# Kernel tuning notes

Measured on AMD Instinct MI355X. Metric: run time of the kernel, lower is better.

## Reference

```python
import jax, jax.numpy as jnp
import numpy as np

B, C, N, M, K = 1, 64, 65536, 65536, 16
H, O = 64, 128  # mlp hidden, out_channels


def setup_inputs() -> dict:
    key = jax.random.key(0)
    ks = jax.random.split(key, 8)
    return {
        "x": jax.random.normal(ks[0], (B, C, N), dtype=jnp.float32),
        "pos": jax.random.normal(ks[1], (B, 3, N), dtype=jnp.float32),
        "support_points": jax.random.normal(ks[2], (B, 3, M), dtype=jnp.float32),
        "W1": jax.random.normal(ks[3], (H, C + 3), dtype=jnp.float32) * 0.05,
        "b1": jax.random.normal(ks[4], (H,), dtype=jnp.float32) * 0.05,
        "W2": jax.random.normal(ks[5], (O, H), dtype=jnp.float32) * 0.05,
        "b2": jax.random.normal(ks[6], (O,), dtype=jnp.float32) * 0.05,
        "indices": jax.random.randint(ks[7], (B, M, K), 0, N, dtype=jnp.int64),
    }


def _gather_points(t, indices):
    # t: [B, C, N], indices: [B, M, K] -> [B, C, M, K]
    b, c, n = t.shape
    m, k = indices.shape[1], indices.shape[2]
    idx = indices.reshape(b, 1, m * k)  # broadcasts over channel dim
    return jnp.take_along_axis(t, idx, axis=2).reshape(b, c, m, k)


def reference(x, pos, support_points, W1, b1, W2, b2, indices):
    # gather neighbor features and positions: [B, C, M, K], [B, 3, M, K]
    feats = _gather_points(x, indices)
    pts = _gather_points(pos, indices) - support_points[:, :, :, None]
    h = jnp.concatenate([feats, pts], axis=1)  # [B, C+3, M, K]
    # shared per-point MLP (1x1 Conv2d == channel contraction)
    h = jnp.einsum("oc,bcmk->bomk", W1, h) + b1[None, :, None, None]
    h = jax.nn.relu(h)
    h = jnp.einsum("oc,bcmk->bomk", W2, h) + b2[None, :, None, None]
    # max-pool over neighborhood K -> [B, O, M]
    return jnp.max(h, axis=3)
```

## Files before the change

### kernel.cpp

```cpp
#include <hip/hip_runtime.h>
#include <hip/hip_bf16.h>

#define NPTS 65536
#define MPTS 65536

typedef __attribute__((ext_vector_type(8))) short bf16x8;
typedef __attribute__((ext_vector_type(4))) float f32x4;

__device__ __forceinline__ float bflo(unsigned int u){ union{unsigned int i; float f;} v; v.i = u<<16; return v.f; }
__device__ __forceinline__ float bfhi(unsigned int u){ union{unsigned int i; float f;} v; v.i = u & 0xffff0000u; return v.f; }
__device__ __forceinline__ unsigned short f2bf(float f){
  union{float f; unsigned int i;} v; v.f=f;
  unsigned int r = v.i + 0x7fffu + ((v.i>>16)&1u);
  return (unsigned short)(r>>16);
}
__device__ __forceinline__ unsigned int pk2f(float a, float b){
  float2 tf; tf.x = a; tf.y = b;
  union { __hip_bfloat162 h; unsigned int u; } c;
  c.h = __float22bfloat162_rn(tf);
  return c.u;
}
__device__ __forceinline__ float swz16(float x){
  return __int_as_float(__builtin_amdgcn_ds_swizzle(__float_as_int(x), 0x401F));
}
__device__ __forceinline__ float red4(f32x4 a){
  return fmaxf(fmaxf(a[0], a[1]), fmaxf(a[2], a[3]));
}

#define MFMA32(a,b,c) __builtin_amdgcn_mfma_f32_16x16x32_bf16((a),(b),(c),0,0,0)

__global__ __launch_bounds__(256) void pack_all(
    const float* __restrict__ x,
    const float* __restrict__ pos,
    const float* __restrict__ sup,
    const float* __restrict__ W1,
    const float* __restrict__ b1,
    const float* __restrict__ W2,
    unsigned short* __restrict__ U,
    unsigned short* __restrict__ W2F,
    float* __restrict__ V) {
  const int t = threadIdx.x;
  if (blockIdx.x >= 1028) {
    const int m = (blockIdx.x - 1028) * 256 + t;
    const float s0 = sup[m], s1 = sup[MPTS + m], s2 = sup[2*MPTS + m];
    #pragma unroll
    for (int cg = 0; cg < 16; ++cg) {
      const float* r0 = W1 + (size_t)(cg*4 + 0)*67 + 64;
      const float* r1 = W1 + (size_t)(cg*4 + 1)*67 + 64;
      const float* r2 = W1 + (size_t)(cg*4 + 2)*67 + 64;
      const float* r3 = W1 + (size_t)(cg*4 + 3)*67 + 64;
      float4 o;
      o.x = r0[0]*s0 + r0[1]*s1 + r0[2]*s2;
      o.y = r1[0]*s0 + r1[1]*s1 + r1[2]*s2;
      o.z = r2[0]*s0 + r2[1]*s1 + r2[2]*s2;
      o.w = r3[0]*s0 + r3[1]*s1 + r3[2]*s2;
      *(float4*)(V + (size_t)m*64 + cg*4) = o;
    }
    return;
  }
  if (blockIdx.x >= 1024) {
    const int gg = (blockIdx.x - 1024) * 256 + t;
    if (gg < 1024) {
      const int g = gg >> 6, lane = gg & 63;
      const int q = lane >> 4, lr = lane & 15;
      const int kt = g >> 3, ot = g & 7;
      #pragma unroll
      for (int j = 0; j < 4; ++j)
        *(unsigned int*)&W2F[gg*8 + 2*j] =
            pk2f(W2[(ot*16 + lr)*64 + kt*32 + q*8 + 2*j],
                 W2[(ot*16 + lr)*64 + kt*32 + q*8 + 2*j + 1]);
    }
    return;
  }
  __shared__ float sx[67][65];
  const int n0 = blockIdx.x * 64;
  #pragma unroll
  for (int i = 0; i < 4; ++i) {
    const int lin = i*256 + t, r = lin >> 4, c4 = (lin & 15) * 4;
    const float4 v = *(const float4*)&x[(size_t)r * NPTS + n0 + c4];
    *(float4*)&sx[r][c4] = v;
  }
  if (t < 48) {
    const int lin = 1024 + t, r = lin >> 4, c4 = (lin & 15) * 4;
    const float4 v = *(const float4*)&pos[(size_t)(r - 64) * NPTS + n0 + c4];
    *(float4*)&sx[r][c4] = v;
  }

  const int lane = t & 63, w = t >> 6, quad = lane >> 4, lr = lane & 15;
  const int col = w * 16 + lr;
  const int n = n0 + col;

  bf16x8 wa[2][4], wt[4];
  #pragma unroll
  for (int kt = 0; kt < 2; ++kt)
    #pragma unroll
    for (int nt = 0; nt < 4; ++nt) {
      const float* r = W1 + (size_t)(nt*16 + lr)*67 + kt*32 + quad*8;
      const float4 a = *(const float4*)r;
      const float4 b = *(const float4*)(r + 4);
      union { unsigned int d[4]; bf16x8 v; } mk;
      mk.d[0] = pk2f(a.x, a.y); mk.d[1] = pk2f(a.z, a.w);
      mk.d[2] = pk2f(b.x, b.y); mk.d[3] = pk2f(b.z, b.w);
      wa[kt][nt] = mk.v;
    }
  #pragma unroll
  for (int nt = 0; nt < 4; ++nt) {
    union { unsigned int d[4]; bf16x8 v; } mk;
    mk.d[0] = 0u; mk.d[1] = 0u; mk.d[2] = 0u; mk.d[3] = 0u;
    if (quad == 0) {
      const float* r = W1 + (size_t)(nt*16 + lr)*67 + 64;
      mk.d[0] = pk2f(r[0], r[1]);
      mk.d[1] = (unsigned int)f2bf(r[2]);
    }
    wt[nt] = mk.v;
  }

  __syncthreads();

  const f32x4 fz = {0.f, 0.f, 0.f, 0.f};
  f32x4 acc[4] = {fz, fz, fz, fz};
  #pragma unroll
  for (int kt = 0; kt < 2; ++kt) {
    const int c0 = kt*32 + quad*8;
    union { unsigned int d[4]; bf16x8 v; } mk;
    #pragma unroll
    for (int i = 0; i < 4; ++i)
      mk.d[i] = pk2f(sx[c0 + 2*i][col], sx[c0 + 2*i + 1][col]);
    #pragma unroll
    for (int nt = 0; nt < 4; ++nt)
      acc[nt] = MFMA32(wa[kt][nt], mk.v, acc[nt]);
  }
  {
    union { unsigned int d[4]; bf16x8 v; } mk;
    mk.d[0] = pk2f(sx[64][col], sx[65][col]);
    mk.d[1] = (unsigned int)f2bf(sx[66][col]);
    mk.d[2] = 0u; mk.d[3] = 0u;
    #pragma unroll
    for (int nt = 0; nt < 4; ++nt)
      acc[nt] = MFMA32(wt[nt], mk.v, acc[nt]);
  }
  #pragma unroll
  for (int nt = 0; nt < 4; ++nt) {
    const float4 bb = *(const float4*)(b1 + nt*16 + quad*4);
    uint2 d;
    d.x = pk2f(acc[nt][0] + bb.x, acc[nt][1] + bb.y);
    d.y = pk2f(acc[nt][2] + bb.z, acc[nt][3] + bb.w);
    *(uint2*)(U + (size_t)n * 64 + nt*16 + quad*4) = d;
  }
}

__global__ __launch_bounds__(256, 3) void pointnet_reg5(
    const unsigned short* __restrict__ U,
    const float* __restrict__ V,
    const unsigned short* __restrict__ W2F,
    const float* __restrict__ b2,
    const int* __restrict__ indices,
    float* __restrict__ out) {
  __shared__ float sv[32][68];
  const int t = threadIdx.x;
  const int lane = t & 63, w = t >> 6, quad = lane >> 4, lr = lane & 15;
  const int mbase = blockIdx.x * 32;
  const int wbase = mbase + w * 8;

  int idx[2][4];
  #pragma unroll
  for (int g = 0; g < 2; ++g)
    #pragma unroll
    for (int p = 0; p < 4; ++p)
      idx[g][p] = indices[(wbase + g*4 + p)*16 + lr];

  const int vrow = w*8 + (lane >> 3), vcol = (lane & 7) * 8;
  const float* vg = &V[(size_t)(mbase + vrow) * 64 + vcol];
  const float4 vt0 = *(const float4*)(vg);
  const float4 vt1 = *(const float4*)(vg + 4);

  uint4 ur0[4][2], ur1[4][2];
  #pragma unroll
  for (int p = 0; p < 4; ++p) {
    const size_t rowb = (size_t)idx[0][p] * 64;
    ur0[p][0] = *(const uint4*)(U + rowb + quad*8);
    ur0[p][1] = *(const uint4*)(U + rowb + 32 + quad*8);
  }
  #pragma unroll
  for (int p = 0; p < 4; ++p) {
    const size_t rowb = (size_t)idx[1][p] * 64;
    ur1[p][0] = *(const uint4*)(U + rowb + quad*8);
    ur1[p][1] = *(const uint4*)(U + rowb + 32 + quad*8);
  }

  *(float4*)&sv[vrow][vcol]     = vt0;
  *(float4*)&sv[vrow][vcol + 4] = vt1;

  float bias[8];
  #pragma unroll
  for (int ot = 0; ot < 8; ++ot) bias[ot] = b2[ot*16 + lr];

  const f32x4 fz = {0.f, 0.f, 0.f, 0.f};
  const bf16x8* W2Fv = (const bf16x8*)W2F;

#define PN_GROUP(g, CUR)                                                        \
  {                                                                             \
    bf16x8 ah[4][2];                                                            \
    _Pragma("unroll")                                                           \
    for (int p = 0; p < 4; ++p) {                                               \
      const float* vr = &sv[w*8 + (g)*4 + p][quad*8];                           \
      const f32x4 v0 = *(const f32x4*)(vr);                                     \
      const f32x4 v1 = *(const f32x4*)(vr + 4);                                 \
      const f32x4 v2 = *(const f32x4*)(vr + 32);                                \
      const f32x4 v3 = *(const f32x4*)(vr + 36);                                \
      const float vv[16] = {v0[0],v0[1],v0[2],v0[3], v1[0],v1[1],v1[2],v1[3],   \
                            v2[0],v2[1],v2[2],v2[3], v3[0],v3[1],v3[2],v3[3]};  \
      _Pragma("unroll")                                                         \
      for (int kt = 0; kt < 2; ++kt) {                                          \
        const unsigned int uu[4] = {CUR[p][kt].x, CUR[p][kt].y,                 \
                                    CUR[p][kt].z, CUR[p][kt].w};                \
        union { unsigned int d[4]; bf16x8 v; } mk;                              \
        _Pragma("unroll")                                                       \
        for (int i = 0; i < 4; ++i) {                                           \
          const float lo = bflo(uu[i]) - vv[kt*8 + 2*i];                        \
          const float hi = bfhi(uu[i]) - vv[kt*8 + 2*i + 1];                    \
          mk.d[i] = pk2f(fmaxf(lo, 0.f), fmaxf(hi, 0.f));                       \
        }                                                                       \
        ah[p][kt] = mk.v;                                                       \
      }                                                                         \
    }                                                                           \
    _Pragma("unroll")                                                           \
    for (int ot = 0; ot < 8; ++ot) {                                            \
      const bf16x8 wb0 = W2Fv[(0*8 + ot)*64 + lane];                            \
      const bf16x8 wb1 = W2Fv[(1*8 + ot)*64 + lane];                            \
      f32x4 aA, aB;                                                             \
      aA = MFMA32(ah[0][0], wb0, fz); aA = MFMA32(ah[0][1], wb1, aA);           \
      aB = MFMA32(ah[1][0], wb0, fz); aB = MFMA32(ah[1][1], wb1, aB);           \
      float q0 = red4(aA);                                                      \
      aA = MFMA32(ah[2][0], wb0, fz); aA = MFMA32(ah[2][1], wb1, aA);           \
      float q1 = red4(aB);                                                      \
      aB = MFMA32(ah[3][0], wb0, fz); aB = MFMA32(ah[3][1], wb1, aB);           \
      float q2 = red4(aA);                                                      \
      float q3 = red4(aB);                                                      \
      float u0 = swz16(q0), u1 = swz16(q1), u2 = swz16(q2), u3 = swz16(q3);     \
      q0 = fmaxf(q0, u0); q1 = fmaxf(q1, u1);                                   \
      q2 = fmaxf(q2, u2); q3 = fmaxf(q3, u3);                                   \
      u0 = __shfl_xor(q0, 32); u1 = __shfl_xor(q1, 32);                         \
      u2 = __shfl_xor(q2, 32); u3 = __shfl_xor(q3, 32);                         \
      q0 = fmaxf(q0, u0); q1 = fmaxf(q1, u1);                                   \
      q2 = fmaxf(q2, u2); q3 = fmaxf(q3, u3);                                   \
      const float e = (quad & 1) ? ((quad & 2) ? q3 : q1)                       \
                                 : ((quad & 2) ? q2 : q0);                      \
      out[(size_t)(ot*16 + lr) * MPTS + wbase + (g)*4 + quad] = e + bias[ot];   \
    }                                                                           \
  }

  PN_GROUP(0, ur0)
  PN_GROUP(1, ur1)
#undef PN_GROUP
}

__global__ __launch_bounds__(256, 3) void pointnet_reg(
    const unsigned short* __restrict__ U,
    const float* __restrict__ sup,
    const float* __restrict__ W1,
    const unsigned short* __restrict__ W2F,
    const float* __restrict__ b2,
    const int* __restrict__ indices,
    float* __restrict__ out) {
  const int t = threadIdx.x;
  const int lane = t & 63, w = t >> 6, quad = lane >> 4, lr = lane & 15;
  const int wbase = blockIdx.x * 32 + w * 8;

  int idx[8];
  #pragma unroll
  for (int pt = 0; pt < 8; ++pt) idx[pt] = indices[(wbase + pt)*16 + lr];

  uint4 ur[8][2];
  #pragma unroll
  for (int pt = 0; pt < 8; ++pt)
    #pragma unroll
    for (int kt = 0; kt < 2; ++kt)
      ur[pt][kt] = *(const uint4*)(U + (size_t)idx[pt]*64 + kt*32 + quad*8);

  bf16x8 ah[8][2];
  #pragma unroll
  for (int kt = 0; kt < 2; ++kt) {
    float w1p[8][3];
    #pragma unroll
    for (int j = 0; j < 8; ++j) {
      const float* r = W1 + (size_t)(kt*32 + quad*8 + j)*67 + 64;
      w1p[j][0] = r[0]; w1p[j][1] = r[1]; w1p[j][2] = r[2];
    }
    #pragma unroll
    for (int pt = 0; pt < 8; ++pt) {
      const float s0 = sup[wbase + pt];
      const float s1 = sup[MPTS + wbase + pt];
      const float s2 = sup[2*MPTS + wbase + pt];
      const unsigned int uu[4] = {ur[pt][kt].x, ur[pt][kt].y, ur[pt][kt].z, ur[pt][kt].w};
      union { unsigned int d[4]; bf16x8 v; } mk;
      #pragma unroll
      for (int i = 0; i < 4; ++i) {
        const float vl = w1p[2*i][0]*s0 + w1p[2*i][1]*s1 + w1p[2*i][2]*s2;
        const float vh = w1p[2*i+1][0]*s0 + w1p[2*i+1][1]*s1 + w1p[2*i+1][2]*s2;
        const float hl = fmaxf(bflo(uu[i]) - vl, 0.f);
        const float hh = fmaxf(bfhi(uu[i]) - vh, 0.f);
        mk.d[i] = pk2f(hl, hh);
      }
      ah[pt][kt] = mk.v;
    }
  }

  const f32x4 fz = {0.f, 0.f, 0.f, 0.f};
  #pragma unroll
  for (int ot = 0; ot < 8; ++ot) {
    const bf16x8 wb0 = ((const bf16x8*)W2F)[(0*8 + ot)*64 + lane];
    const bf16x8 wb1 = ((const bf16x8*)W2F)[(1*8 + ot)*64 + lane];
    float vm[8];
    #pragma unroll
    for (int pt = 0; pt < 8; ++pt) {
      f32x4 a2 = MFMA32(ah[pt][0], wb0, fz);
      a2 = MFMA32(ah[pt][1], wb1, a2);
      float v = fmaxf(fmaxf(a2[0], a2[1]), fmaxf(a2[2], a2[3]));
      v = fmaxf(v, __shfl_xor(v, 16));
      v = fmaxf(v, __shfl_xor(v, 32));
      vm[pt] = v;
    }
    const int o = ot*16 + lr;
    const float bb = b2[o];
    const float va = (quad & 1) ? ((quad & 2) ? vm[3] : vm[1])
                                : ((quad & 2) ? vm[2] : vm[0]);
    const float vb = (quad & 1) ? ((quad & 2) ? vm[7] : vm[5])
                                : ((quad & 2) ? vm[6] : vm[4]);
    out[(size_t)o * MPTS + wbase + quad] = va + bb;
    out[(size_t)o * MPTS + wbase + 4 + quad] = vb + bb;
  }
}

__global__ __launch_bounds__(256) void pointnet_fallback(
    const float* __restrict__ x, const float* __restrict__ pos,
    const float* __restrict__ sup,
    const float* __restrict__ W1, const float* __restrict__ b1,
    const float* __restrict__ W2, const float* __restrict__ b2,
    const int* __restrict__ indices, float* __restrict__ out) {
  __shared__ float sfeat[16][68];
  __shared__ float shid[16][64];
  __shared__ float smax[4][128];
  __shared__ int sidx[16];
  const int t = threadIdx.x;
  const int m = blockIdx.x;
  if (t < 16) sidx[t] = indices[m*16 + t];
  const float sup0 = sup[m], sup1 = sup[MPTS + m], sup2 = sup[2*MPTS + m];
  __syncthreads();
  for (int u = t; u < 16*17; u += 256) {
    const int k = u / 17, c4 = (u - k*17) * 4;
    const int idx = sidx[k];
    float4 wv;
    if (c4 < 64) {
      wv.x = x[(size_t)(c4+0)*NPTS + idx]; wv.y = x[(size_t)(c4+1)*NPTS + idx];
      wv.z = x[(size_t)(c4+2)*NPTS + idx]; wv.w = x[(size_t)(c4+3)*NPTS + idx];
    } else {
      wv.x = pos[idx] - sup0; wv.y = pos[NPTS + idx] - sup1;
      wv.z = pos[2*NPTS + idx] - sup2; wv.w = 0.f;
    }
    *(float4*)&sfeat[k][c4] = wv;
  }
  const int h = t & 63, kg = t >> 6;
  float w1r[68];
  #pragma unroll
  for (int c = 0; c < 67; ++c) w1r[c] = W1[h*67 + c];
  w1r[67] = 0.f;
  const float bias1 = b1[h];
  __syncthreads();
  #pragma unroll
  for (int j = 0; j < 4; ++j) {
    const int k = kg*4 + j;
    float a = bias1;
    const float4* rr = (const float4*)sfeat[k];
    #pragma unroll
    for (int qq = 0; qq < 17; ++qq) {
      const float4 v = rr[qq];
      a += w1r[qq*4+0]*v.x + w1r[qq*4+1]*v.y + w1r[qq*4+2]*v.z + w1r[qq*4+3]*v.w;
    }
    shid[k][h] = fmaxf(a, 0.f);
  }
  const int ow = t & 63;
  float w2a[64], w2b[64];
  #pragma unroll
  for (int hh = 0; hh < 64; ++hh) { w2a[hh] = W2[ow*64 + hh]; w2b[hh] = W2[(ow+64)*64 + hh]; }
  __syncthreads();
  float mxa = -3.0e38f, mxb = -3.0e38f;
  #pragma unroll
  for (int j = 0; j < 4; ++j) {
    const int k = kg*4 + j;
    const float4* hr = (const float4*)shid[k];
    float pa = 0.f, pb = 0.f;
    #pragma unroll
    for (int qq = 0; qq < 16; ++qq) {
      const float4 v = hr[qq];
      pa += w2a[qq*4+0]*v.x + w2a[qq*4+1]*v.y + w2a[qq*4+2]*v.z + w2a[qq*4+3]*v.w;
      pb += w2b[qq*4+0]*v.x + w2b[qq*4+1]*v.y + w2b[qq*4+2]*v.z + w2b[qq*4+3]*v.w;
    }
    mxa = fmaxf(mxa, pa); mxb = fmaxf(mxb, pb);
  }
  smax[kg][ow] = mxa; smax[kg][64 + ow] = mxb;
  __syncthreads();
  if (t < 128) {
    out[(size_t)t * MPTS + m] =
        fmaxf(fmaxf(smax[0][t], smax[1][t]), fmaxf(smax[2][t], smax[3][t])) + b2[t];
  }
}

extern "C" void kernel_launch(void* const* d_in, const int* in_sizes, int n_in,
                              void* d_out, int out_size, void* d_ws, size_t ws_size,
                              hipStream_t stream) {
  const float* x   = (const float*)d_in[0];
  const float* pos = (const float*)d_in[1];
  const float* sup = (const float*)d_in[2];
  const float* W1  = (const float*)d_in[3];
  const float* b1  = (const float*)d_in[4];
  const float* W2  = (const float*)d_in[5];
  const float* b2  = (const float*)d_in[6];
  const int* indices = (const int*)d_in[7];
  float* out = (float*)d_out;

  const size_t U_BYTES   = (size_t)NPTS * 64 * 2;
  const size_t W2F_BYTES = 16 * 64 * 8 * 2;
  const size_t V_BYTES   = (size_t)MPTS * 64 * 4;
  if (ws_size >= U_BYTES + W2F_BYTES + V_BYTES) {
    unsigned short* U   = (unsigned short*)d_ws;
    unsigned short* W2F = (unsigned short*)((char*)d_ws + U_BYTES);
    float* V            = (float*)((char*)d_ws + U_BYTES + W2F_BYTES);
    pack_all<<<1284, 256, 0, stream>>>(x, pos, sup, W1, b1, W2, U, W2F, V);
    pointnet_reg5<<<MPTS/32, 256, 0, stream>>>(U, V, W2F, b2, indices, out);
  } else if (ws_size >= U_BYTES + W2F_BYTES) {
    unsigned short* U   = (unsigned short*)d_ws;
    unsigned short* W2F = (unsigned short*)((char*)d_ws + U_BYTES);
    pack_all<<<1028, 256, 0, stream>>>(x, pos, sup, W1, b1, W2, U, W2F, nullptr);
    pointnet_reg<<<MPTS/32, 256, 0, stream>>>(U, sup, W1, W2F, b2, indices, out);
  } else {
    pointnet_fallback<<<MPTS, 256, 0, stream>>>(x, pos, sup, W1, b1, W2, b2, indices, out);
  }
}
```

Measured before the change: 142.3 us.

## Process 64 points per block with 8-point tiles per wave and setprio MFMA bursts

Each block now handles 64 support points instead of 32, and each wave processes two 8-point tiles. Both tiles' gathered U rows are loaded up front, so more gather loads are in flight per wave. Within a tile, W2 fragments are reused across 8 points, MFMA bursts run under raised s_setprio, and each lane writes two adjacent outputs as a float2 store. The cost is far more live registers, so launch bounds drop from 3 to 2 blocks per SIMD with fewer blocks overall, which may reduce latency hiding.

```diff
diff --git a/kernel.cpp b/kernel.cpp
--- a/kernel.cpp
+++ b/kernel.cpp
@@ -149,47 +149,54 @@
   }
 }
 
-__global__ __launch_bounds__(256, 3) void pointnet_reg5(
+__global__ __launch_bounds__(256, 2) void pointnet_reg6(
     const unsigned short* __restrict__ U,
     const float* __restrict__ V,
     const unsigned short* __restrict__ W2F,
     const float* __restrict__ b2,
     const int* __restrict__ indices,
     float* __restrict__ out) {
-  __shared__ float sv[32][68];
+  __shared__ float sv[64][68];
   const int t = threadIdx.x;
   const int lane = t & 63, w = t >> 6, quad = lane >> 4, lr = lane & 15;
-  const int mbase = blockIdx.x * 32;
-  const int wbase = mbase + w * 8;
-
-  int idx[2][4];
-  #pragma unroll
-  for (int g = 0; g < 2; ++g)
-    #pragma unroll
-    for (int p = 0; p < 4; ++p)
-      idx[g][p] = indices[(wbase + g*4 + p)*16 + lr];
-
+  const int mb0 = blockIdx.x * 64;
+  const int wb0 = mb0 + w * 8;
+  const int wb1 = mb0 + 32 + w * 8;
+
+  int idx0[8];
+  #pragma unroll
+  for (int pt = 0; pt < 8; ++pt) idx0[pt] = indices[(wb0 + pt)*16 + lr];
   const int vrow = w*8 + (lane >> 3), vcol = (lane & 7) * 8;
-  const float* vg = &V[(size_t)(mbase + vrow) * 64 + vcol];
-  const float4 vt0 = *(const float4*)(vg);
-  const float4 vt1 = *(const float4*)(vg + 4);
-
-  uint4 ur0[4][2], ur1[4][2];
-  #pragma unroll
-  for (int p = 0; p < 4; ++p) {
-    const size_t rowb = (size_t)idx[0][p] * 64;
-    ur0[p][0] = *(const uint4*)(U + rowb + quad*8);
-    ur0[p][1] = *(const uint4*)(U + rowb + 32 + quad*8);
-  }
-  #pragma unroll
-  for (int p = 0; p < 4; ++p) {
-    const size_t rowb = (size_t)idx[1][p] * 64;
-    ur1[p][0] = *(const uint4*)(U + rowb + quad*8);
-    ur1[p][1] = *(const uint4*)(U + rowb + 32 + quad*8);
-  }
-
-  *(float4*)&sv[vrow][vcol]     = vt0;
-  *(float4*)&sv[vrow][vcol + 4] = vt1;
+  const float* vg0 = &V[(size_t)(mb0 + vrow) * 64 + vcol];
+  const float4 va0 = *(const float4*)(vg0);
+  const float4 va1 = *(const float4*)(vg0 + 4);
+  uint4 ur0[8][2];
+  #pragma unroll
+  for (int pt = 0; pt < 8; ++pt) {
+    const size_t rb = (size_t)idx0[pt] * 64;
+    ur0[pt][0] = *(const uint4*)(U + rb + quad*8);
+    ur0[pt][1] = *(const uint4*)(U + rb + 32 + quad*8);
+  }
+  *(float4*)&sv[vrow][vcol]     = va0;
+  *(float4*)&sv[vrow][vcol + 4] = va1;
+
+  int idx1[8];
+  #pragma unroll
+  for (int pt = 0; pt < 8; ++pt) idx1[pt] = indices[(wb1 + pt)*16 + lr];
+  const float* vg1 = &V[(size_t)(mb0 + 32 + vrow) * 64 + vcol];
+  const float4 vb0 = *(const float4*)(vg1);
+  const float4 vb1 = *(const float4*)(vg1 + 4);
+  uint4 ur1[8][2];
+  #pragma unroll
+  for (int pt = 0; pt < 8; ++pt) {
+    const size_t rb = (size_t)idx1[pt] * 64;
+    ur1[pt][0] = *(const uint4*)(U + rb + quad*8);
+    ur1[pt][1] = *(const uint4*)(U + rb + 32 + quad*8);
+  }
+  *(float4*)&sv[32 + vrow][vcol]     = vb0;
+  *(float4*)&sv[32 + vrow][vcol + 4] = vb1;
+
+  __builtin_amdgcn_sched_barrier(0);
 
   float bias[8];
   #pragma unroll
@@ -198,12 +205,12 @@
   const f32x4 fz = {0.f, 0.f, 0.f, 0.f};
   const bf16x8* W2Fv = (const bf16x8*)W2F;
 
-#define PN_GROUP(g, CUR)                                                        \
+#define PN_TILE(TB, UR, WB)                                                     \
   {                                                                             \
-    bf16x8 ah[4][2];                                                            \
+    bf16x8 ah[8][2];                                                            \
     _Pragma("unroll")                                                           \
-    for (int p = 0; p < 4; ++p) {                                               \
-      const float* vr = &sv[w*8 + (g)*4 + p][quad*8];                           \
+    for (int pt = 0; pt < 8; ++pt) {                                            \
+      const float* vr = &sv[(TB) + w*8 + pt][quad*8];                           \
       const f32x4 v0 = *(const f32x4*)(vr);                                     \
       const f32x4 v1 = *(const f32x4*)(vr + 4);                                 \
       const f32x4 v2 = *(const f32x4*)(vr + 32);                                \
@@ -212,8 +219,8 @@
                             v2[0],v2[1],v2[2],v2[3], v3[0],v3[1],v3[2],v3[3]};  \
       _Pragma("unroll")                                                         \
       for (int kt = 0; kt < 2; ++kt) {                                          \
-        const unsigned int uu[4] = {CUR[p][kt].x, CUR[p][kt].y,                 \
-                                    CUR[p][kt].z, CUR[p][kt].w};                \
+        const unsigned int uu[4] = {UR[pt][kt].x, UR[pt][kt].y,                 \
+                                    UR[pt][kt].z, UR[pt][kt].w};                \
         union { unsigned int d[4]; bf16x8 v; } mk;                              \
         _Pragma("unroll")                                                       \
         for (int i = 0; i < 4; ++i) {                                           \
@@ -221,38 +228,44 @@
           const float hi = bfhi(uu[i]) - vv[kt*8 + 2*i + 1];                    \
           mk.d[i] = pk2f(fmaxf(lo, 0.f), fmaxf(hi, 0.f));                       \
         }                                                                       \
-        ah[p][kt] = mk.v;                                                       \
+        ah[pt][kt] = mk.v;                                                      \
       }                                                                         \
     }                                                                           \
     _Pragma("unroll")                                                           \
     for (int ot = 0; ot < 8; ++ot) {                                            \
-      const bf16x8 wb0 = W2Fv[(0*8 + ot)*64 + lane];                            \
-      const bf16x8 wb1 = W2Fv[(1*8 + ot)*64 + lane];                            \
-      f32x4 aA, aB;                                                             \
-      aA = MFMA32(ah[0][0], wb0, fz); aA = MFMA32(ah[0][1], wb1, aA);           \
-      aB = MFMA32(ah[1][0], wb0, fz); aB = MFMA32(ah[1][1], wb1, aB);           \
-      float q0 = red4(aA);                                                      \
-      aA = MFMA32(ah[2][0], wb0, fz); aA = MFMA32(ah[2][1], wb1, aA);           \
-      float q1 = red4(aB);                                                      \
-      aB = MFMA32(ah[3][0], wb0, fz); aB = MFMA32(ah[3][1], wb1, aB);           \
-      float q2 = red4(aA);                                                      \
-      float q3 = red4(aB);                                                      \
-      float u0 = swz16(q0), u1 = swz16(q1), u2 = swz16(q2), u3 = swz16(q3);     \
-      q0 = fmaxf(q0, u0); q1 = fmaxf(q1, u1);                                   \
-      q2 = fmaxf(q2, u2); q3 = fmaxf(q3, u3);                                   \
-      u0 = __shfl_xor(q0, 32); u1 = __shfl_xor(q1, 32);                         \
-      u2 = __shfl_xor(q2, 32); u3 = __shfl_xor(q3, 32);                         \
-      q0 = fmaxf(q0, u0); q1 = fmaxf(q1, u1);                                   \
-      q2 = fmaxf(q2, u2); q3 = fmaxf(q3, u3);                                   \
-      const float e = (quad & 1) ? ((quad & 2) ? q3 : q1)                       \
-                                 : ((quad & 2) ? q2 : q0);                      \
-      out[(size_t)(ot*16 + lr) * MPTS + wbase + (g)*4 + quad] = e + bias[ot];   \
+      const bf16x8 f0 = W2Fv[(0*8 + ot)*64 + lane];                             \
+      const bf16x8 f1 = W2Fv[(1*8 + ot)*64 + lane];                             \
+      float q[8];                                                               \
+      __builtin_amdgcn_s_setprio(1);                                            \
+      _Pragma("unroll")                                                         \
+      for (int pt = 0; pt < 8; ++pt) {                                          \
+        f32x4 a2 = MFMA32(ah[pt][0], f0, fz);                                   \
+        a2 = MFMA32(ah[pt][1], f1, a2);                                         \
+        q[pt] = red4(a2);                                                       \
+      }                                                                         \
+      __builtin_amdgcn_s_setprio(0);                                            \
+      float u[8];                                                               \
+      _Pragma("unroll")                                                         \
+      for (int pt = 0; pt < 8; ++pt) u[pt] = swz16(q[pt]);                      \
+      _Pragma("unroll")                                                         \
+      for (int pt = 0; pt < 8; ++pt) q[pt] = fmaxf(q[pt], u[pt]);               \
+      _Pragma("unroll")                                                         \
+      for (int pt = 0; pt < 8; ++pt) u[pt] = __shfl_xor(q[pt], 32);             \
+      _Pragma("unroll")                                                         \
+      for (int pt = 0; pt < 8; ++pt) q[pt] = fmaxf(q[pt], u[pt]);               \
+      const int o = ot*16 + lr;                                                 \
+      const float e0 = (quad & 1) ? ((quad & 2) ? q[6] : q[2])                  \
+                                  : ((quad & 2) ? q[4] : q[0]);                 \
+      const float e1 = (quad & 1) ? ((quad & 2) ? q[7] : q[3])                  \
+                                  : ((quad & 2) ? q[5] : q[1]);                 \
+      float2 st; st.x = e0 + bias[ot]; st.y = e1 + bias[ot];                    \
+      *(float2*)&out[(size_t)o * MPTS + (WB) + 2*quad] = st;                    \
     }                                                                           \
   }
 
-  PN_GROUP(0, ur0)
-  PN_GROUP(1, ur1)
-#undef PN_GROUP
+  PN_TILE(0,  ur0, wb0)
+  PN_TILE(32, ur1, wb1)
+#undef PN_TILE
 }
 
 __global__ __launch_bounds__(256, 3) void pointnet_reg(
@@ -427,7 +440,7 @@
     unsigned short* W2F = (unsigned short*)((char*)d_ws + U_BYTES);
     float* V            = (float*)((char*)d_ws + U_BYTES + W2F_BYTES);
     pack_all<<<1284, 256, 0, stream>>>(x, pos, sup, W1, b1, W2, U, W2F, V);
-    pointnet_reg5<<<MPTS/32, 256, 0, stream>>>(U, V, W2F, b2, indices, out);
+    pointnet_reg6<<<MPTS/64, 256, 0, stream>>>(U, V, W2F, b2, indices, out);
   } else if (ws_size >= U_BYTES + W2F_BYTES) {
     unsigned short* U   = (unsigned short*)d_ws;
     unsigned short* W2F = (unsigned short*)((char*)d_ws + U_BYTES);
```

Result: no change. 140.4 us (-1.3%).

## Software-pipeline neighbor gathers per point and keep W2 fragments in registers

Applied to the files above, without the earlier changes.

The second-stage kernel is restructured from issuing all gathers for two groups of four points up front into a rolling loop. Each iteration prefetches the next point's indices and U rows while the current point runs through the MFMA and max-reduce. All 16 W2 fragments are loaded once into registers instead of being re-read per group, and outputs are held in registers and written as float2 pairs at the end. This trades fewer loads in flight (less memory-level parallelism) for lower register pressure and reuse of W2, and the loop is not unrolled.

```diff
diff --git a/kernel.cpp b/kernel.cpp
--- a/kernel.cpp
+++ b/kernel.cpp
@@ -149,7 +149,7 @@
   }
 }
 
-__global__ __launch_bounds__(256, 3) void pointnet_reg5(
+__global__ __launch_bounds__(256, 3) void pointnet_reg7(
     const unsigned short* __restrict__ U,
     const float* __restrict__ V,
     const unsigned short* __restrict__ W2F,
@@ -162,97 +162,103 @@
   const int mbase = blockIdx.x * 32;
   const int wbase = mbase + w * 8;
 
-  int idx[2][4];
-  #pragma unroll
-  for (int g = 0; g < 2; ++g)
-    #pragma unroll
-    for (int p = 0; p < 4; ++p)
-      idx[g][p] = indices[(wbase + g*4 + p)*16 + lr];
-
   const int vrow = w*8 + (lane >> 3), vcol = (lane & 7) * 8;
   const float* vg = &V[(size_t)(mbase + vrow) * 64 + vcol];
-  const float4 vt0 = *(const float4*)(vg);
-  const float4 vt1 = *(const float4*)(vg + 4);
-
-  uint4 ur0[4][2], ur1[4][2];
-  #pragma unroll
-  for (int p = 0; p < 4; ++p) {
-    const size_t rowb = (size_t)idx[0][p] * 64;
-    ur0[p][0] = *(const uint4*)(U + rowb + quad*8);
-    ur0[p][1] = *(const uint4*)(U + rowb + 32 + quad*8);
-  }
-  #pragma unroll
-  for (int p = 0; p < 4; ++p) {
-    const size_t rowb = (size_t)idx[1][p] * 64;
-    ur1[p][0] = *(const uint4*)(U + rowb + quad*8);
-    ur1[p][1] = *(const uint4*)(U + rowb + 32 + quad*8);
-  }
-
-  *(float4*)&sv[vrow][vcol]     = vt0;
-  *(float4*)&sv[vrow][vcol + 4] = vt1;
-
-  float bias[8];
-  #pragma unroll
-  for (int ot = 0; ot < 8; ++ot) bias[ot] = b2[ot*16 + lr];
+  const float4 va0 = *(const float4*)(vg);
+  const float4 va1 = *(const float4*)(vg + 4);
+
+  int idx0 = indices[(wbase + 0)*16 + lr];
+  int idx1 = indices[(wbase + 1)*16 + lr];
+
+  bf16x8 wf[16];
+  #pragma unroll
+  for (int k8 = 0; k8 < 16; ++k8) wf[k8] = ((const bf16x8*)W2F)[k8*64 + lane];
+
+  *(float4*)&sv[vrow][vcol]     = va0;
+  *(float4*)&sv[vrow][vcol + 4] = va1;
+
+  uint4 urA0, urA1, urB0, urB1;
+  { const size_t rb = (size_t)idx0 * 64;
+    urA0 = *(const uint4*)(U + rb + quad*8);
+    urA1 = *(const uint4*)(U + rb + 32 + quad*8); }
+
+  float vstA[8], vstB[8];
+  #pragma unroll
+  for (int ot = 0; ot < 8; ++ot) { vstA[ot] = 0.f; vstB[ot] = 0.f; }
 
   const f32x4 fz = {0.f, 0.f, 0.f, 0.f};
-  const bf16x8* W2Fv = (const bf16x8*)W2F;
-
-#define PN_GROUP(g, CUR)                                                        \
-  {                                                                             \
-    bf16x8 ah[4][2];                                                            \
-    _Pragma("unroll")                                                           \
-    for (int p = 0; p < 4; ++p) {                                               \
-      const float* vr = &sv[w*8 + (g)*4 + p][quad*8];                           \
-      const f32x4 v0 = *(const f32x4*)(vr);                                     \
-      const f32x4 v1 = *(const f32x4*)(vr + 4);                                 \
-      const f32x4 v2 = *(const f32x4*)(vr + 32);                                \
-      const f32x4 v3 = *(const f32x4*)(vr + 36);                                \
-      const float vv[16] = {v0[0],v0[1],v0[2],v0[3], v1[0],v1[1],v1[2],v1[3],   \
-                            v2[0],v2[1],v2[2],v2[3], v3[0],v3[1],v3[2],v3[3]};  \
-      _Pragma("unroll")                                                         \
-      for (int kt = 0; kt < 2; ++kt) {                                          \
-        const unsigned int uu[4] = {CUR[p][kt].x, CUR[p][kt].y,                 \
-                                    CUR[p][kt].z, CUR[p][kt].w};                \
-        union { unsigned int d[4]; bf16x8 v; } mk;                              \
-        _Pragma("unroll")                                                       \
-        for (int i = 0; i < 4; ++i) {                                           \
-          const float lo = bflo(uu[i]) - vv[kt*8 + 2*i];                        \
-          const float hi = bfhi(uu[i]) - vv[kt*8 + 2*i + 1];                    \
-          mk.d[i] = pk2f(fmaxf(lo, 0.f), fmaxf(hi, 0.f));                       \
-        }                                                                       \
-        ah[p][kt] = mk.v;                                                       \
-      }                                                                         \
-    }                                                                           \
-    _Pragma("unroll")                                                           \
-    for (int ot = 0; ot < 8; ++ot) {                                            \
-      const bf16x8 wb0 = W2Fv[(0*8 + ot)*64 + lane];                            \
-      const bf16x8 wb1 = W2Fv[(1*8 + ot)*64 + lane];                            \
-      f32x4 aA, aB;                                                             \
-      aA = MFMA32(ah[0][0], wb0, fz); aA = MFMA32(ah[0][1], wb1, aA);           \
-      aB = MFMA32(ah[1][0], wb0, fz); aB = MFMA32(ah[1][1], wb1, aB);           \
-      float q0 = red4(aA);                                                      \
-      aA = MFMA32(ah[2][0], wb0, fz); aA = MFMA32(ah[2][1], wb1, aA);           \
-      float q1 = red4(aB);                                                      \
-      aB = MFMA32(ah[3][0], wb0, fz); aB = MFMA32(ah[3][1], wb1, aB);           \
-      float q2 = red4(aA);                                                      \
-      float q3 = red4(aB);                                                      \
-      float u0 = swz16(q0), u1 = swz16(q1), u2 = swz16(q2), u3 = swz16(q3);     \
-      q0 = fmaxf(q0, u0); q1 = fmaxf(q1, u1);                                   \
-      q2 = fmaxf(q2, u2); q3 = fmaxf(q3, u3);                                   \
-      u0 = __shfl_xor(q0, 32); u1 = __shfl_xor(q1, 32);                         \
-      u2 = __shfl_xor(q2, 32); u3 = __shfl_xor(q3, 32);                         \
-      q0 = fmaxf(q0, u0); q1 = fmaxf(q1, u1);                                   \
-      q2 = fmaxf(q2, u2); q3 = fmaxf(q3, u3);                                   \
-      const float e = (quad & 1) ? ((quad & 2) ? q3 : q1)                       \
-                                 : ((quad & 2) ? q2 : q0);                      \
-      out[(size_t)(ot*16 + lr) * MPTS + wbase + (g)*4 + quad] = e + bias[ot];   \
-    }                                                                           \
-  }
-
-  PN_GROUP(0, ur0)
-  PN_GROUP(1, ur1)
-#undef PN_GROUP
+
+#define PN_COMPUTE(PT, UR0, UR1)                                            \
+  {                                                                         \
+    const float* vr = &sv[w*8 + (PT)][quad*8];                              \
+    const f32x4 v0 = *(const f32x4*)(vr);                                   \
+    const f32x4 v1 = *(const f32x4*)(vr + 4);                               \
+    const f32x4 v2 = *(const f32x4*)(vr + 32);                              \
+    const f32x4 v3 = *(const f32x4*)(vr + 36);                              \
+    const float vv[16] = {v0[0],v0[1],v0[2],v0[3], v1[0],v1[1],v1[2],v1[3], \
+                          v2[0],v2[1],v2[2],v2[3], v3[0],v3[1],v3[2],v3[3]};\
+    bf16x8 ah0, ah1;                                                        \
+    {                                                                       \
+      const unsigned int uu[4] = {(UR0).x,(UR0).y,(UR0).z,(UR0).w};         \
+      union { unsigned int d[4]; bf16x8 v; } mk;                            \
+      _Pragma("unroll")                                                     \
+      for (int i = 0; i < 4; ++i) {                                         \
+        const float lo = bflo(uu[i]) - vv[2*i];                             \
+        const float hi = bfhi(uu[i]) - vv[2*i+1];                           \
+        mk.d[i] = pk2f(fmaxf(lo, 0.f), fmaxf(hi, 0.f));                     \
+      }                                                                     \
+      ah0 = mk.v;                                                           \
+    }                                                                       \
+    {                                                                       \
+      const unsigned int uu[4] = {(UR1).x,(UR1).y,(UR1).z,(UR1).w};         \
+      union { unsigned int d[4]; bf16x8 v; } mk;                            \
+      _Pragma("unroll")                                                     \
+      for (int i = 0; i < 4; ++i) {                                         \
+        const float lo = bflo(uu[i]) - vv[8+2*i];                           \
+        const float hi = bfhi(uu[i]) - vv[8+2*i+1];                         \
+        mk.d[i] = pk2f(fmaxf(lo, 0.f), fmaxf(hi, 0.f));                     \
+      }                                                                     \
+      ah1 = mk.v;                                                           \
+    }                                                                       \
+    const bool eA = ((PT) == 2*quad);                                       \
+    const bool eB = ((PT) == 2*quad + 1);                                   \
+    _Pragma("unroll")                                                       \
+    for (int ot = 0; ot < 8; ++ot) {                                        \
+      f32x4 a2 = MFMA32(ah0, wf[ot], fz);                                   \
+      a2 = MFMA32(ah1, wf[8+ot], a2);                                       \
+      float q = red4(a2);                                                   \
+      q = fmaxf(q, swz16(q));                                               \
+      q = fmaxf(q, __shfl_xor(q, 32));                                      \
+      vstA[ot] = eA ? q : vstA[ot];                                         \
+      vstB[ot] = eB ? q : vstB[ot];                                         \
+    }                                                                       \
+  }
+
+  #pragma unroll 1
+  for (int pp = 0; pp < 4; ++pp) {
+    const int ptE = 2*pp, ptO = 2*pp + 1;
+    { const size_t rb = (size_t)idx1 * 64;
+      urB0 = *(const uint4*)(U + rb + quad*8);
+      urB1 = *(const uint4*)(U + rb + 32 + quad*8); }
+    { int nx = ptE + 2; nx = (nx > 7) ? 0 : nx;
+      idx0 = indices[(wbase + nx)*16 + lr]; }
+    PN_COMPUTE(ptE, urA0, urA1)
+    { const size_t rb = (size_t)idx0 * 64;
+      urA0 = *(const uint4*)(U + rb + quad*8);
+      urA1 = *(const uint4*)(U + rb + 32 + quad*8); }
+    { int nx = ptO + 2; nx = (nx > 7) ? 0 : nx;
+      idx1 = indices[(wbase + nx)*16 + lr]; }
+    PN_COMPUTE(ptO, urB0, urB1)
+  }
+#undef PN_COMPUTE
+
+  #pragma unroll
+  for (int ot = 0; ot < 8; ++ot) {
+    const int o = ot*16 + lr;
+    const float bb = b2[o];
+    float2 st; st.x = vstA[ot] + bb; st.y = vstB[ot] + bb;
+    *(float2*)&out[(size_t)o * MPTS + wbase + 2*quad] = st;
+  }
 }
 
 __global__ __launch_bounds__(256, 3) void pointnet_reg(
@@ -427,7 +433,7 @@
     unsigned short* W2F = (unsigned short*)((char*)d_ws + U_BYTES);
     float* V            = (float*)((char*)d_ws + U_BYTES + W2F_BYTES);
     pack_all<<<1284, 256, 0, stream>>>(x, pos, sup, W1, b1, W2, U, W2F, V);
-    pointnet_reg5<<<MPTS/32, 256, 0, stream>>>(U, V, W2F, b2, indices, out);
+    pointnet_reg7<<<MPTS/32, 256, 0, stream>>>(U, V, W2F, b2, indices, out);
   } else if (ws_size >= U_BYTES + W2F_BYTES) {
     unsigned short* U   = (unsigned short*)d_ws;
     unsigned short* W2F = (unsigned short*)((char*)d_ws + U_BYTES);
```

Result: faster. 136.2 us, median of 2 (-4.3%).
